# Kernel tuning notes

Hardware: AMD Instinct MI355X
Metric: run time of the kernel (lower is better)

Reference implementation:

```python
import jax, jax.numpy as jnp
import numpy as np

N, E, B, D, L, IN, H = 50000, 800000, 64, 64, 4, 7, 4


def _leaky(x, s=0.2):
    return jnp.where(x >= 0, x, s * x)


def _layernorm(x, g, b, eps=1e-5):
    mu = x.mean(-1, keepdims=True)
    v = ((x - mu) ** 2).mean(-1, keepdims=True)
    return (x - mu) * jax.lax.rsqrt(v + eps) * g + b


def _forward(x, edge_index, batch,
             enc_W, enc_b,
             gat_Wl, gat_Wr, gat_att, gat_b,
             ln_g, ln_b, ffn_W1, ffn_b1, ffn_W2, ffn_b2,
             n2g_W1, n2g_b1, n2g_W2, n2g_b2,
             g2n_W1, g2n_b1, g2n_W2, g2n_b2,
             dec_W1, dec_b1, dec_W2, dec_b2):
    n = x.shape[0]
    loops = jnp.arange(n, dtype=edge_index.dtype)
    src = jnp.concatenate([edge_index[0], loops])  # PyG add_self_loops=True
    dst = jnp.concatenate([edge_index[1], loops])

    h = x @ enc_W + enc_b  # encoder [N, D]
    for l in range(L):
        # ---- GATv2Conv(heads=4, concat=False), eval mode (dropout off) ----
        xl = (h @ gat_Wl[l]).reshape(n, H, D)  # source transform (lin_l)
        xr = (h @ gat_Wr[l]).reshape(n, H, D)  # target transform (lin_r)
        s = xl[src] + xr[dst]                              # [Et, H, D]
        e = jnp.sum(_leaky(s) * gat_att[l], axis=-1)       # [Et, H]
        m = jax.ops.segment_max(e, dst, num_segments=n)
        a = jnp.exp(e - m[dst])
        denom = jax.ops.segment_sum(a, dst, num_segments=n)
        a = a / (denom[dst] + 1e-16)                       # segment softmax
        out = jax.ops.segment_sum(a[..., None] * xl[src], dst, num_segments=n)
        out = out.mean(axis=1) + gat_b[l]                  # head average + bias
        # ---- residual + LayerNorm + FFN ----
        h2 = _layernorm(h + out, ln_g[l], ln_b[l])
        h = h2 + (_leaky(h2 @ ffn_W1[l] + ffn_b1[l]) @ ffn_W2[l] + ffn_b2[l])
        # ---- GlobalContextLayer ----
        lat = jax.nn.gelu(h @ n2g_W1[l] + n2g_b1[l]) @ n2g_W2[l] + n2g_b2[l]
        cnt = jax.ops.segment_sum(jnp.ones((n, 1), h.dtype), batch, num_segments=B)
        gmean = jax.ops.segment_sum(lat, batch, num_segments=B) / jnp.maximum(cnt, 1.0)
        gmax = jax.ops.segment_max(lat, batch, num_segments=B)
        gl = jnp.concatenate([gmean, gmax], axis=1)        # [B, 2D]
        ctx = jax.nn.gelu(gl @ g2n_W1[l] + g2n_b1[l]) @ g2n_W2[l] + g2n_b2[l]
        h = h + ctx[batch]
    return jax.nn.gelu(h @ dec_W1 + dec_b1) @ dec_W2 + dec_b2  # [N, 2]


def setup_inputs() -> dict:
    key = jax.random.key(0)
    ks = jax.random.split(key, 16)
    f = lambda i, s: jax.random.normal(ks[i], s, dtype=jnp.float32) * 0.1
    z = lambda s: jnp.zeros(s, jnp.float32)
    return dict(
        x=jax.random.normal(ks[0], (N, IN), dtype=jnp.float32),
        edge_index=jax.random.randint(ks[1], (2, E), 0, N, dtype=jnp.int32),
        batch=jnp.sort(jax.random.randint(ks[2], (N,), 0, B, dtype=jnp.int32)),
        enc_W=f(3, (IN, D)), enc_b=z((D,)),
        gat_Wl=f(4, (L, D, H * D)), gat_Wr=f(5, (L, D, H * D)),
        gat_att=f(6, (L, H, D)), gat_b=z((L, D)),
        ln_g=jnp.ones((L, D), jnp.float32), ln_b=z((L, D)),
        ffn_W1=f(7, (L, D, 2 * D)), ffn_b1=z((L, 2 * D)),
        ffn_W2=f(8, (L, 2 * D, D)), ffn_b2=z((L, D)),
        n2g_W1=f(9, (L, D, D)), n2g_b1=z((L, D)),
        n2g_W2=f(10, (L, D, D)), n2g_b2=z((L, D)),
        g2n_W1=f(11, (L, 2 * D, D)), g2n_b1=z((L, D)),
        g2n_W2=f(12, (L, D, D)), g2n_b2=z((L, D)),
        dec_W1=f(13, (D, D)), dec_b1=z((D,)),
        dec_W2=f(14, (D, 2)), dec_b2=z((2,)),
    )


def reference(x, edge_index, batch, enc_W, enc_b, gat_Wl, gat_Wr, gat_att, gat_b,
              ln_g, ln_b, ffn_W1, ffn_b1, ffn_W2, ffn_b2,
              n2g_W1, n2g_b1, n2g_W2, n2g_b2,
              g2n_W1, g2n_b1, g2n_W2, g2n_b2,
              dec_W1, dec_b1, dec_W2, dec_b2):
    return _forward(x, edge_index, batch, enc_W, enc_b, gat_Wl, gat_Wr, gat_att, gat_b,
                    ln_g, ln_b, ffn_W1, ffn_b1, ffn_W2, ffn_b2,
                    n2g_W1, n2g_b1, n2g_W2, n2g_b2,
                    g2n_W1, g2n_b1, g2n_W2, g2n_b2,
                    dec_W1, dec_b1, dec_W2, dec_b2)
```

## Files before the change

kernel.cpp:

```cpp
#include <hip/hip_runtime.h>
#include <hip/hip_bf16.h>
#include <math.h>

#define NN 50000
#define EE 800000
#define BBATCH 64
#define DDIM 64
#define NLAYER 4
#define NIN 7
#define NHEAD 4

typedef __attribute__((ext_vector_type(8))) short short8v;
typedef __attribute__((ext_vector_type(4))) float f32x4;

static __device__ __forceinline__ float wave_sum(float v) {
#pragma unroll
  for (int m = 32; m > 0; m >>= 1) v += __shfl_xor(v, m, 64);
  return v;
}

static __device__ __forceinline__ float gelu_t(float x) {
  float z = 0.7978845608f * (x + 0.044715f * x * x * x);
  float t = 2.f / (1.f + __expf(-2.f * z)) - 1.f;
  return 0.5f * x * (1.f + t);
}

static __device__ __forceinline__ unsigned short f2b(float v) {
  __hip_bfloat16 b = __float2bfloat16(v);
  return *reinterpret_cast<unsigned short*>(&b);
}

static __device__ __forceinline__ unsigned fkey(float x) {
  unsigned u = __builtin_bit_cast(unsigned, x);
  return (u >> 31) ? ~u : (u | 0x80000000u);
}
static __device__ __forceinline__ float fkey_inv(unsigned k) {
  unsigned u = (k & 0x80000000u) ? (k ^ 0x80000000u) : ~k;
  return __builtin_bit_cast(float, u);
}

template <int CTRL>
static __device__ __forceinline__ float dppf(float v) {
  int x = __builtin_amdgcn_mov_dpp(__builtin_bit_cast(int, v), CTRL, 0xF, 0xF, true);
  return __builtin_bit_cast(float, x);
}

static __device__ __forceinline__ void unpack8(uint4 u, float* xs) {
  unsigned int w[4] = {u.x, u.y, u.z, u.w};
#pragma unroll
  for (int k = 0; k < 4; k++) {
    xs[2 * k]     = __builtin_bit_cast(float, w[k] << 16);
    xs[2 * k + 1] = __builtin_bit_cast(float, w[k] & 0xFFFF0000u);
  }
}

__global__ void k_init_cnt(int* cnt, int n) {
  int i = blockIdx.x * blockDim.x + threadIdx.x;
  if (i < n) cnt[i] = 1;
}

__global__ void k_count_edges(const int* __restrict__ dst, int e, int* cnt) {
  int i = blockIdx.x * blockDim.x + threadIdx.x;
  if (i < e) atomicAdd(&cnt[dst[i]], 1);
}

__global__ void k_scan_bsum(const int* __restrict__ cnt, int n, int* bsum) {
  __shared__ int red[256];
  int b = blockIdx.x, t = threadIdx.x;
  int s = 0;
  for (int i = b * 1024 + t; i < (b + 1) * 1024; i += 256)
    if (i < n) s += cnt[i];
  red[t] = s;
  __syncthreads();
  for (int o = 128; o > 0; o >>= 1) {
    if (t < o) red[t] += red[t + o];
    __syncthreads();
  }
  if (t == 0) bsum[b] = red[0];
}

__global__ void k_scan_offsets(int* bsum, int nb) {
  if (threadIdx.x == 0 && blockIdx.x == 0) {
    int acc = 0;
    for (int i = 0; i < nb; i++) { int v = bsum[i]; bsum[i] = acc; acc += v; }
  }
}

__global__ void k_scan_final(const int* __restrict__ cnt, int n,
                             const int* __restrict__ bsum, int* indptr) {
  __shared__ int lds[256];
  int b = blockIdx.x, t = threadIdx.x;
  int base = b * 1024;
  int v[4];
  int s = 0;
#pragma unroll
  for (int j = 0; j < 4; j++) {
    int i = base + t * 4 + j;
    v[j] = (i < n) ? cnt[i] : 0;
    s += v[j];
  }
  lds[t] = s;
  __syncthreads();
  for (int o = 1; o < 256; o <<= 1) {
    int x = (t >= o) ? lds[t - o] : 0;
    __syncthreads();
    lds[t] += x;
    __syncthreads();
  }
  int run = bsum[b] + lds[t] - s;
#pragma unroll
  for (int j = 0; j < 4; j++) {
    int i = base + t * 4 + j;
    if (i <= n) indptr[i] = run;
    run += v[j];
  }
}

__global__ void k_csr_self(const int* __restrict__ indptr, int* nxt, int* esrc, int n) {
  int i = blockIdx.x * blockDim.x + threadIdx.x;
  if (i < n) {
    int p = indptr[i];
    esrc[p] = i;
    nxt[i] = p + 1;
  }
}

__global__ void k_csr_fill(const int* __restrict__ src, const int* __restrict__ dst,
                           int e, int* nxt, int* esrc) {
  int i = blockIdx.x * blockDim.x + threadIdx.x;
  if (i < e) {
    int p = atomicAdd(&nxt[dst[i]], 1);
    esrc[p] = src[i];
  }
}

__global__ void k_batch_starts(const int* __restrict__ batch, int n, int nb, int* starts) {
  int i = blockIdx.x * blockDim.x + threadIdx.x;
  if (i >= n) return;
  int b = batch[i];
  if (i == 0) {
    for (int x = 0; x <= b; x++) starts[x] = 0;
  } else {
    int pb = batch[i - 1];
    if (pb != b)
      for (int x = pb + 1; x <= b; x++) starts[x] = i;
  }
  if (i == n - 1) {
    for (int x = b + 1; x <= nb; x++) starts[x] = n;
  }
}

#define SEG_LR (4 * 512 * 64)
#define SEG_F1 (4 * 128 * 64)
#define SEG_F2 (4 * 64 * 128)
#define SEG_N  (4 * 64 * 64)
#define SEG_D  (64 * 64)
#define WPREP_TOTAL (SEG_LR + SEG_F1 + SEG_F2 + 2 * SEG_N + SEG_D)
__global__ void k_wprep_all(const float* __restrict__ Wl, const float* __restrict__ Wr,
                            const float* __restrict__ F1, const float* __restrict__ F2,
                            const float* __restrict__ N1, const float* __restrict__ N2,
                            const float* __restrict__ D1,
                            unsigned short* __restrict__ wLR, unsigned short* __restrict__ wF1,
                            unsigned short* __restrict__ wF2, unsigned short* __restrict__ wN1,
                            unsigned short* __restrict__ wN2, unsigned short* __restrict__ wD1) {
  int idx = blockIdx.x * blockDim.x + threadIdx.x;
  if (idx < SEG_LR) {
    int l = idx / (512 * 64), rem = idx % (512 * 64);
    int c = rem / 64, k = rem % 64;
    float v = (c < 256) ? Wl[(size_t)l * 64 * 256 + k * 256 + c]
                        : Wr[(size_t)l * 64 * 256 + k * 256 + (c - 256)];
    wLR[idx] = f2b(v);
    return;
  }
  idx -= SEG_LR;
  if (idx < SEG_F1) {
    int l = idx / (128 * 64), rem = idx % (128 * 64);
    int c = rem / 64, k = rem % 64;
    wF1[idx] = f2b(F1[(size_t)l * 64 * 128 + k * 128 + c]);
    return;
  }
  idx -= SEG_F1;
  if (idx < SEG_F2) {
    int l = idx / (64 * 128), rem = idx % (64 * 128);
    int c = rem / 128, k = rem % 128;
    wF2[idx] = f2b(F2[(size_t)l * 128 * 64 + k * 64 + c]);
    return;
  }
  idx -= SEG_F2;
  if (idx < SEG_N) {
    int l = idx / (64 * 64), rem = idx % (64 * 64);
    int c = rem / 64, k = rem % 64;
    wN1[idx] = f2b(N1[(size_t)l * 64 * 64 + k * 64 + c]);
    return;
  }
  idx -= SEG_N;
  if (idx < SEG_N) {
    int l = idx / (64 * 64), rem = idx % (64 * 64);
    int c = rem / 64, k = rem % 64;
    wN2[idx] = f2b(N2[(size_t)l * 64 * 64 + k * 64 + c]);
    return;
  }
  idx -= SEG_N;
  if (idx < SEG_D) {
    int c = idx / 64, k = idx % 64;
    wD1[idx] = f2b(D1[k * 64 + c]);
  }
}

__global__ void k_encoder(const float* __restrict__ x, const float* __restrict__ W,
                          const float* __restrict__ bias, float* __restrict__ h,
                          unsigned short* __restrict__ hb, int n) {
  int idx = blockIdx.x * blockDim.x + threadIdx.x;
  if (idx >= n * 64) return;
  int i = idx >> 6, d = idx & 63;
  float acc = bias[d];
#pragma unroll
  for (int k = 0; k < NIN; k++) acc += x[i * NIN + k] * W[k * 64 + d];
  h[idx] = acc;
  hb[idx] = f2b(acc);
}

template <int K, int ACT, bool RES, bool BIAS, bool OUTF, bool OUTB>
__global__ __launch_bounds__(256) void k_mgemm(const unsigned short* __restrict__ A,
                                               const unsigned short* __restrict__ Wt,
                                               const float* __restrict__ bias,
                                               const float* __restrict__ res,
                                               float* __restrict__ C,
                                               unsigned short* __restrict__ Cb,
                                               int n, int Co) {
  constexpr int NF = K / 32;
  const int lane = threadIdx.x & 63, wave = threadIdx.x >> 6;
  const int row0 = blockIdx.x * 64 + wave * 16;
  const int c0 = blockIdx.y * 64;
  const int karow = (lane >> 4) * 8;
  const int arow = row0 + (lane & 15);
  const size_t abase = (size_t)(arow < n ? arow : 0) * K + karow;

  short8v a[NF];
#pragma unroll
  for (int f = 0; f < NF; f++)
    a[f] = *(const short8v*)(A + abase + f * 32);

  f32x4 acc[4];
#pragma unroll
  for (int cc = 0; cc < 4; cc++) {
    const int c = c0 + cc * 16 + (lane & 15);
    f32x4 t = {0.f, 0.f, 0.f, 0.f};
#pragma unroll
    for (int f = 0; f < NF; f++) {
      short8v b = *(const short8v*)(Wt + (size_t)c * K + f * 32 + karow);
      t = __builtin_amdgcn_mfma_f32_16x16x32_bf16(a[f], b, t, 0, 0, 0);
    }
    acc[cc] = t;
  }

#pragma unroll
  for (int cc = 0; cc < 4; cc++) {
    const int c = c0 + cc * 16 + (lane & 15);
    const float bv = BIAS ? bias[c] : 0.f;
#pragma unroll
    for (int r = 0; r < 4; r++) {
      const int row = row0 + (lane >> 4) * 4 + r;
      if (row < n) {
        float v = acc[cc][r] + bv;
        if (ACT == 1) v = fmaxf(v, 0.2f * v);
        else if (ACT == 2) v = gelu_t(v);
        if (RES) v += res[(size_t)row * Co + c];
        if (OUTF) C[(size_t)row * Co + c] = v;
        if (OUTB) Cb[(size_t)row * Co + c] = f2b(v);
      }
    }
  }
}

__global__ __launch_bounds__(256) void k_ffn(const unsigned short* __restrict__ A,
                                             const unsigned short* __restrict__ W1t,
                                             const float* __restrict__ b1,
                                             const unsigned short* __restrict__ W2t,
                                             const float* __restrict__ b2,
                                             const float* __restrict__ res,
                                             float* __restrict__ C,
                                             unsigned short* __restrict__ Cb, int n) {
  __shared__ unsigned short tl[4][16 * 136];
  const int lane = threadIdx.x & 63, wave = threadIdx.x >> 6;
  const int row0 = blockIdx.x * 64 + wave * 16;
  const int karow = (lane >> 4) * 8;
  const int arow = row0 + (lane & 15);
  const size_t abase = (size_t)(arow < n ? arow : 0) * 64 + karow;
  short8v a0 = *(const short8v*)(A + abase);
  short8v a1 = *(const short8v*)(A + abase + 32);

#pragma unroll
  for (int cc = 0; cc < 8; cc++) {
    const int c = cc * 16 + (lane & 15);
    f32x4 t = {0.f, 0.f, 0.f, 0.f};
    t = __builtin_amdgcn_mfma_f32_16x16x32_bf16(a0, *(const short8v*)(W1t + (size_t)c * 64 + karow), t, 0, 0, 0);
    t = __builtin_amdgcn_mfma_f32_16x16x32_bf16(a1, *(const short8v*)(W1t + (size_t)c * 64 + 32 + karow), t, 0, 0, 0);
    const float bv = b1[c];
#pragma unroll
    for (int r = 0; r < 4; r++) {
      float v = t[r] + bv;
      v = fmaxf(v, 0.2f * v);
      int rr = (lane >> 4) * 4 + r;
      tl[wave][rr * 136 + c] = f2b(v);
    }
  }
  __syncthreads();

  short8v a2[4];
#pragma unroll
  for (int f = 0; f < 4; f++)
    a2[f] = *(const short8v*)(&tl[wave][(lane & 15) * 136 + f * 32 + karow]);

#pragma unroll
  for (int cc = 0; cc < 4; cc++) {
    const int c = cc * 16 + (lane & 15);
    f32x4 t = {0.f, 0.f, 0.f, 0.f};
#pragma unroll
    for (int f = 0; f < 4; f++)
      t = __builtin_amdgcn_mfma_f32_16x16x32_bf16(a2[f], *(const short8v*)(W2t + (size_t)c * 128 + f * 32 + karow), t, 0, 0, 0);
    const float bv = b2[c];
#pragma unroll
    for (int r = 0; r < 4; r++) {
      const int row = row0 + (lane >> 4) * 4 + r;
      if (row < n) {
        float v = t[r] + bv + res[(size_t)row * 64 + c];
        C[(size_t)row * 64 + c] = v;
        Cb[(size_t)row * 64 + c] = f2b(v);
      }
    }
  }
}

__global__ __launch_bounds__(256) void k_n2g(const unsigned short* __restrict__ A,
                                             const unsigned short* __restrict__ W1t,
                                             const float* __restrict__ b1,
                                             const unsigned short* __restrict__ W2t,
                                             const float* __restrict__ b2,
                                             const int* __restrict__ batch,
                                             float* __restrict__ psum,
                                             unsigned int* __restrict__ pmax, int n) {
  __shared__ unsigned short tl[4][16 * 72];
  __shared__ float s_sum[64];
  __shared__ unsigned s_max[64];
  const int lane = threadIdx.x & 63, wave = threadIdx.x >> 6;
  const int row0b = blockIdx.x * 64;
  const int row0 = row0b + wave * 16;
  const int karow = (lane >> 4) * 8;
  const int arow = row0 + (lane & 15);
  const size_t abase = (size_t)(arow < n ? arow : 0) * 64 + karow;
  if (threadIdx.x < 64) { s_sum[threadIdx.x] = 0.f; s_max[threadIdx.x] = 0u; }
  short8v a0 = *(const short8v*)(A + abase);
  short8v a1 = *(const short8v*)(A + abase + 32);

#pragma unroll
  for (int cc = 0; cc < 4; cc++) {
    const int c = cc * 16 + (lane & 15);
    f32x4 t = {0.f, 0.f, 0.f, 0.f};
    t = __builtin_amdgcn_mfma_f32_16x16x32_bf16(a0, *(const short8v*)(W1t + (size_t)c * 64 + karow), t, 0, 0, 0);
    t = __builtin_amdgcn_mfma_f32_16x16x32_bf16(a1, *(const short8v*)(W1t + (size_t)c * 64 + 32 + karow), t, 0, 0, 0);
    const float bv = b1[c];
#pragma unroll
    for (int r = 0; r < 4; r++) {
      int rr = (lane >> 4) * 4 + r;
      tl[wave][rr * 72 + c] = f2b(gelu_t(t[r] + bv));
    }
  }
  __syncthreads();

  short8v a2[2];
#pragma unroll
  for (int f = 0; f < 2; f++)
    a2[f] = *(const short8v*)(&tl[wave][(lane & 15) * 72 + f * 32 + karow]);

  float pv[4][4];
#pragma unroll
  for (int cc = 0; cc < 4; cc++) {
    const int c = cc * 16 + (lane & 15);
    f32x4 t = {0.f, 0.f, 0.f, 0.f};
    t = __builtin_amdgcn_mfma_f32_16x16x32_bf16(a2[0], *(const short8v*)(W2t + (size_t)c * 64 + karow), t, 0, 0, 0);
    t = __builtin_amdgcn_mfma_f32_16x16x32_bf16(a2[1], *(const short8v*)(W2t + (size_t)c * 64 + 32 + karow), t, 0, 0, 0);
    const float bv = b2[c];
#pragma unroll
    for (int r = 0; r < 4; r++) pv[cc][r] = t[r] + bv;
  }

  const int blo = batch[row0b];
  const int last = row0b + 63 < n ? row0b + 63 : n - 1;
  const int bhi = batch[last];
  if (blo == bhi && row0b + 63 < n) {
#pragma unroll
    for (int cc = 0; cc < 4; cc++) {
      const int c = cc * 16 + (lane & 15);
      float s = pv[cc][0] + pv[cc][1] + pv[cc][2] + pv[cc][3];
      float mx = fmaxf(fmaxf(pv[cc][0], pv[cc][1]), fmaxf(pv[cc][2], pv[cc][3]));
      atomicAdd(&s_sum[c], s);
      atomicMax(&s_max[c], fkey(mx));
    }
    __syncthreads();
    if (threadIdx.x < 64) {
      atomicAdd(&psum[blo * 64 + threadIdx.x], s_sum[threadIdx.x]);
      atomicMax(&pmax[blo * 64 + threadIdx.x], s_max[threadIdx.x]);
    }
  } else {
#pragma unroll
    for (int cc = 0; cc < 4; cc++) {
      const int c = cc * 16 + (lane & 15);
#pragma unroll
      for (int r = 0; r < 4; r++) {
        const int row = row0 + (lane >> 4) * 4 + r;
        if (row < n) {
          const int b = batch[row];
          atomicAdd(&psum[b * 64 + c], pv[cc][r]);
          atomicMax(&pmax[b * 64 + c], fkey(pv[cc][r]));
        }
      }
    }
  }
}

__global__ __launch_bounds__(256) void k_gat(const unsigned short* __restrict__ xlr,
                                             const float* __restrict__ att,
                                             const float* __restrict__ gbias,
                                             const float* __restrict__ lng,
                                             const float* __restrict__ lnb,
                                             const float* __restrict__ h,
                                             const int* __restrict__ indptr,
                                             const int* __restrict__ esrc,
                                             float* __restrict__ h2,
                                             unsigned short* __restrict__ h2b, int n) {
  const int wave = threadIdx.x >> 6, lane = threadIdx.x & 63;
  const int node = blockIdx.x * 4 + wave;
  if (node >= n) return;
  const int q = lane >> 4, r = lane & 15;
  const int c = r & 3;
  const int doff = (r >> 2) * 64 + c * 16;

  float xr_d[16], att_d[16];
  {
    const uint4* xp = (const uint4*)(xlr + (size_t)node * 512 + 256 + doff);
    uint4 u0 = xp[0], u1 = xp[1];
    unpack8(u0, xr_d);
    unpack8(u1, xr_d + 8);
    const float4* ap = (const float4*)(att + doff);
#pragma unroll
    for (int k = 0; k < 4; k++) {
      float4 a = ap[k];
      att_d[4 * k] = a.x; att_d[4 * k + 1] = a.y;
      att_d[4 * k + 2] = a.z; att_d[4 * k + 3] = a.w;
    }
  }

  float acc[16] = {};
  float den = 0.f;
  const int beg = indptr[node], end = indptr[node + 1];

  int j0 = beg + q;
  int s_cur = esrc[(j0 < end) ? j0 : beg];
  const uint4* xp0 = (const uint4*)(xlr + (size_t)s_cur * 512 + doff);
  uint4 u0 = xp0[0], u1 = xp0[1];
  int jn1 = beg + 4 + q;
  int s_nxt = esrc[(jn1 < end && beg + 4 < end) ? jn1 : beg];

  for (int jb = beg; jb < end; jb += 4) {
    const uint4 cu0 = u0, cu1 = u1;
    const bool cvalid = (jb + q) < end;
    if (jb + 4 < end) {
      const uint4* xpn = (const uint4*)(xlr + (size_t)s_nxt * 512 + doff);
      u0 = xpn[0];
      u1 = xpn[1];
      if (jb + 8 < end) {
        const int jn = jb + 8 + q;
        s_nxt = esrc[(jn < end) ? jn : beg];
      }
    }
    float xs[16];
    unpack8(cu0, xs);
    unpack8(cu1, xs + 8);
    float p0 = 0.f, p1 = 0.f, p2 = 0.f, p3 = 0.f;
#pragma unroll
    for (int k = 0; k < 4; k++) {
      float t0 = xs[4 * k + 0] + xr_d[4 * k + 0]; t0 = fmaxf(t0, 0.2f * t0); p0 = fmaf(t0, att_d[4 * k + 0], p0);
      float t1 = xs[4 * k + 1] + xr_d[4 * k + 1]; t1 = fmaxf(t1, 0.2f * t1); p1 = fmaf(t1, att_d[4 * k + 1], p1);
      float t2 = xs[4 * k + 2] + xr_d[4 * k + 2]; t2 = fmaxf(t2, 0.2f * t2); p2 = fmaf(t2, att_d[4 * k + 2], p2);
      float t3 = xs[4 * k + 3] + xr_d[4 * k + 3]; t3 = fmaxf(t3, 0.2f * t3); p3 = fmaf(t3, att_d[4 * k + 3], p3);
    }
    float p = (p0 + p1) + (p2 + p3);
    p += dppf<0xB1>(p);
    p += dppf<0x4E>(p);
    const float pw = cvalid ? __expf(fminf(p, 60.f)) : 0.f;
    den += pw;
#pragma unroll
    for (int d = 0; d < 16; d++) acc[d] = fmaf(pw, xs[d], acc[d]);
  }

  den += __shfl_xor(den, 16, 64);
  den += __shfl_xor(den, 32, 64);
#pragma unroll
  for (int d = 0; d < 16; d++) {
    acc[d] += __shfl_xor(acc[d], 16, 64);
    acc[d] += __shfl_xor(acc[d], 32, 64);
  }

  const float rden = 0.25f / (den + 1e-16f);
  float y[16];
  float s4 = 0.f;
  const float4* hp = (const float4*)(h + (size_t)node * 64 + c * 16);
  const float4* gp = (const float4*)(gbias + c * 16);
#pragma unroll
  for (int k = 0; k < 4; k++) {
    float4 hv = hp[k], gv = gp[k];
    float hf[4] = {hv.x, hv.y, hv.z, hv.w};
    float gf[4] = {gv.x, gv.y, gv.z, gv.w};
#pragma unroll
    for (int d2 = 0; d2 < 4; d2++) {
      int d = 4 * k + d2;
      float v = acc[d] * rden;
      v += dppf<0x124>(v);
      v += dppf<0x128>(v);
      y[d] = hf[d2] + v + gf[d2];
      s4 += y[d];
    }
  }

  const float mu = wave_sum(s4) * (1.f / 1024.f);
  float v4 = 0.f;
  float dv[16];
#pragma unroll
  for (int d = 0; d < 16; d++) {
    dv[d] = y[d] - mu;
    v4 += dv[d] * dv[d];
  }
  const float var = wave_sum(v4) * (1.f / 1024.f);
  const float rstd = rsqrtf(var + 1e-5f);

  if (lane < 4) {
    float4* outp = (float4*)(h2 + (size_t)node * 64 + lane * 16);
    uint2* outb = (uint2*)(h2b + (size_t)node * 64 + lane * 16);
    const float4* lgp = (const float4*)(lng + lane * 16);
    const float4* lbp = (const float4*)(lnb + lane * 16);
#pragma unroll
    for (int k = 0; k < 4; k++) {
      float4 g = lgp[k], b = lbp[k];
      float o0 = dv[4 * k + 0] * rstd * g.x + b.x;
      float o1 = dv[4 * k + 1] * rstd * g.y + b.y;
      float o2 = dv[4 * k + 2] * rstd * g.z + b.z;
      float o3 = dv[4 * k + 3] * rstd * g.w + b.w;
      float4 of; of.x = o0; of.y = o1; of.z = o2; of.w = o3;
      outp[k] = of;
      uint2 pk;
      pk.x = (unsigned int)f2b(o0) | ((unsigned int)f2b(o1) << 16);
      pk.y = (unsigned int)f2b(o2) | ((unsigned int)f2b(o3) << 16);
      outb[k] = pk;
    }
  }
}

__global__ void k_ctx2(const float* __restrict__ psum, const unsigned int* __restrict__ pmax,
                       const int* __restrict__ starts,
                       const float* __restrict__ W1, const float* __restrict__ b1,
                       const float* __restrict__ W2, const float* __restrict__ b2,
                       float* __restrict__ ctx) {
  int b = blockIdx.x;
  int t = threadIdx.x;
  __shared__ float g[128], tt[64];
  int cnt = starts[b + 1] - starts[b];
  if (t < 64) {
    g[t] = psum[b * 64 + t] / fmaxf((float)cnt, 1.0f);
  } else {
    g[t] = fkey_inv(pmax[b * 64 + (t - 64)]);
  }
  __syncthreads();
  if (t < 64) {
    float acc = b1[t];
    for (int k = 0; k < 128; k++) acc += g[k] * W1[k * 64 + t];
    tt[t] = gelu_t(acc);
  }
  __syncthreads();
  if (t < 64) {
    float acc2 = b2[t];
    for (int k = 0; k < 64; k++) acc2 += tt[k] * W2[k * 64 + t];
    ctx[b * 64 + t] = acc2;
  }
}

__global__ void k_add_ctx(float* __restrict__ h, unsigned short* __restrict__ hb,
                          const float* __restrict__ ctx,
                          const int* __restrict__ batch, int n) {
  int idx = blockIdx.x * blockDim.x + threadIdx.x;
  if (idx >= n * 64) return;
  int i = idx >> 6, d = idx & 63;
  float v = h[idx] + ctx[batch[i] * 64 + d];
  h[idx] = v;
  hb[idx] = f2b(v);
}

__global__ __launch_bounds__(256) void k_dec(const unsigned short* __restrict__ A,
                                             const unsigned short* __restrict__ W1t,
                                             const float* __restrict__ b1,
                                             const float* __restrict__ W2,
                                             const float* __restrict__ b2,
                                             float* __restrict__ out, int n) {
  const int lane = threadIdx.x & 63, wave = threadIdx.x >> 6;
  const int row0 = blockIdx.x * 64 + wave * 16;
  const int karow = (lane >> 4) * 8;
  const int arow = row0 + (lane & 15);
  const size_t abase = (size_t)(arow < n ? arow : 0) * 64 + karow;
  short8v a0 = *(const short8v*)(A + abase);
  short8v a1 = *(const short8v*)(A + abase + 32);

  float o0[4] = {}, o1[4] = {};
#pragma unroll
  for (int cc = 0; cc < 4; cc++) {
    const int cidx = cc * 16 + (lane & 15);
    f32x4 t = {0.f, 0.f, 0.f, 0.f};
    t = __builtin_amdgcn_mfma_f32_16x16x32_bf16(a0, *(const short8v*)(W1t + (size_t)cidx * 64 + karow), t, 0, 0, 0);
    t = __builtin_amdgcn_mfma_f32_16x16x32_bf16(a1, *(const short8v*)(W1t + (size_t)cidx * 64 + 32 + karow), t, 0, 0, 0);
    const float bv = b1[cidx];
    const float w0 = W2[cidx * 2 + 0], w1 = W2[cidx * 2 + 1];
#pragma unroll
    for (int r = 0; r < 4; r++) {
      float v = gelu_t(t[r] + bv);
      o0[r] = fmaf(v, w0, o0[r]);
      o1[r] = fmaf(v, w1, o1[r]);
    }
  }
#pragma unroll
  for (int m = 1; m < 16; m <<= 1) {
#pragma unroll
    for (int r = 0; r < 4; r++) {
      o0[r] += __shfl_xor(o0[r], m, 64);
      o1[r] += __shfl_xor(o1[r], m, 64);
    }
  }
  if ((lane & 15) == 0) {
#pragma unroll
    for (int r = 0; r < 4; r++) {
      const int row = row0 + (lane >> 4) * 4 + r;
      if (row < n) {
        out[2 * row] = o0[r] + b2[0];
        out[2 * row + 1] = o1[r] + b2[1];
      }
    }
  }
}

extern "C" void kernel_launch(void* const* d_in, const int* in_sizes, int n_in,
                              void* d_out, int out_size, void* d_ws, size_t ws_size,
                              hipStream_t stream) {
  const float* x = (const float*)d_in[0];
  const int* ei = (const int*)d_in[1];
  const int* batch = (const int*)d_in[2];
  const float* enc_W = (const float*)d_in[3];
  const float* enc_b = (const float*)d_in[4];
  const float* gat_Wl = (const float*)d_in[5];
  const float* gat_Wr = (const float*)d_in[6];
  const float* gat_att = (const float*)d_in[7];
  const float* gat_b = (const float*)d_in[8];
  const float* ln_g = (const float*)d_in[9];
  const float* ln_b = (const float*)d_in[10];
  const float* ffn_W1 = (const float*)d_in[11];
  const float* ffn_b1 = (const float*)d_in[12];
  const float* ffn_W2 = (const float*)d_in[13];
  const float* ffn_b2 = (const float*)d_in[14];
  const float* n2g_W1 = (const float*)d_in[15];
  const float* n2g_b1 = (const float*)d_in[16];
  const float* n2g_W2 = (const float*)d_in[17];
  const float* n2g_b2 = (const float*)d_in[18];
  const float* g2n_W1 = (const float*)d_in[19];
  const float* g2n_b1 = (const float*)d_in[20];
  const float* g2n_W2 = (const float*)d_in[21];
  const float* g2n_b2 = (const float*)d_in[22];
  const float* dec_W1 = (const float*)d_in[23];
  const float* dec_b1 = (const float*)d_in[24];
  const float* dec_W2 = (const float*)d_in[25];
  const float* dec_b2 = (const float*)d_in[26];

  const int N = NN, E = EE;
  const int* e_src = ei;
  const int* e_dst = ei + E;

  float* h = (float*)d_ws;
  float* h2 = h + (size_t)N * 64;
  float* ctx = h2 + (size_t)N * 64;
  float* psum = ctx + BBATCH * 64;
  unsigned int* pmax = (unsigned int*)(psum + BBATCH * 64);
  int* cnt = (int*)(pmax + BBATCH * 64);
  int* indptr = cnt + N;
  int* esrc = indptr + N + 1;
  int* bsum = esrc + (E + N);
  int* starts = bsum + 64;
  size_t off = (size_t)(starts + BBATCH + 1) - (size_t)d_ws;
  off = (off + 15) & ~(size_t)15;
  unsigned short* hb = (unsigned short*)((char*)d_ws + off);
  unsigned short* h2b = hb + (size_t)N * 64;
  unsigned short* xlr = h2b + (size_t)N * 64;
  unsigned short* wLR = xlr + (size_t)N * 512;
  unsigned short* wF1 = wLR + SEG_LR;
  unsigned short* wF2 = wF1 + SEG_F1;
  unsigned short* wN1 = wF2 + SEG_F2;
  unsigned short* wN2 = wN1 + SEG_N;
  unsigned short* wD1 = wN2 + SEG_N;

  const int TPB = 256;
  const int NBLK_SCAN = (N + 1 + 1023) / 1024;

  hipLaunchKernelGGL(k_wprep_all, dim3((WPREP_TOTAL + 255) / 256), dim3(256), 0, stream,
                     gat_Wl, gat_Wr, ffn_W1, ffn_W2, n2g_W1, n2g_W2, dec_W1,
                     wLR, wF1, wF2, wN1, wN2, wD1);

  hipLaunchKernelGGL(k_init_cnt, dim3((N + TPB - 1) / TPB), dim3(TPB), 0, stream, cnt, N);
  hipLaunchKernelGGL(k_count_edges, dim3((E + TPB - 1) / TPB), dim3(TPB), 0, stream, e_dst, E, cnt);
  hipLaunchKernelGGL(k_scan_bsum, dim3(NBLK_SCAN), dim3(256), 0, stream, cnt, N, bsum);
  hipLaunchKernelGGL(k_scan_offsets, dim3(1), dim3(64), 0, stream, bsum, NBLK_SCAN);
  hipLaunchKernelGGL(k_scan_final, dim3(NBLK_SCAN), dim3(256), 0, stream, cnt, N, bsum, indptr);
  hipLaunchKernelGGL(k_csr_self, dim3((N + TPB - 1) / TPB), dim3(TPB), 0, stream, indptr, cnt, esrc, N);
  hipLaunchKernelGGL(k_csr_fill, dim3((E + TPB - 1) / TPB), dim3(TPB), 0, stream, e_src, e_dst, E, cnt, esrc);
  hipLaunchKernelGGL(k_batch_starts, dim3((N + TPB - 1) / TPB), dim3(TPB), 0, stream, batch, N, BBATCH, starts);

  hipLaunchKernelGGL(k_encoder, dim3((N * 64 + TPB - 1) / TPB), dim3(TPB), 0, stream,
                     x, enc_W, enc_b, h, hb, N);

  const int GN = (N + 63) / 64;

  for (int l = 0; l < NLAYER; l++) {
    const unsigned short* LRt = wLR + (size_t)l * 512 * 64;
    const unsigned short* F1t = wF1 + (size_t)l * 128 * 64;
    const unsigned short* F2t = wF2 + (size_t)l * 64 * 128;
    const unsigned short* N1t = wN1 + (size_t)l * 64 * 64;
    const unsigned short* N2t = wN2 + (size_t)l * 64 * 64;
    const float* attl = gat_att + (size_t)l * 256;
    const float* gbl = gat_b + (size_t)l * 64;
    const float* lngl = ln_g + (size_t)l * 64;
    const float* lnbl = ln_b + (size_t)l * 64;
    const float* fb1 = ffn_b1 + (size_t)l * 128;
    const float* fb2 = ffn_b2 + (size_t)l * 64;
    const float* nb1 = n2g_b1 + (size_t)l * 64;
    const float* nb2 = n2g_b2 + (size_t)l * 64;
    const float* gW1 = g2n_W1 + (size_t)l * 128 * 64;
    const float* gb1 = g2n_b1 + (size_t)l * 64;
    const float* gW2 = g2n_W2 + (size_t)l * 64 * 64;
    const float* gb2 = g2n_b2 + (size_t)l * 64;

    hipLaunchKernelGGL((k_mgemm<64, 0, false, false, false, true>), dim3(GN, 8), dim3(256), 0, stream,
                       hb, LRt, nullptr, nullptr, nullptr, xlr, N, 512);
    hipLaunchKernelGGL(k_gat, dim3((N + 3) / 4), dim3(256), 0, stream,
                       xlr, attl, gbl, lngl, lnbl, h, indptr, esrc, h2, h2b, N);
    hipLaunchKernelGGL(k_ffn, dim3(GN), dim3(256), 0, stream,
                       h2b, F1t, fb1, F2t, fb2, h2, h, hb, N);
    hipMemsetAsync(psum, 0, BBATCH * 64 * (sizeof(float) + sizeof(unsigned int)), stream);
    hipLaunchKernelGGL(k_n2g, dim3(GN), dim3(256), 0, stream,
                       hb, N1t, nb1, N2t, nb2, batch, psum, pmax, N);
    hipLaunchKernelGGL(k_ctx2, dim3(BBATCH), dim3(128), 0, stream,
                       psum, pmax, starts, gW1, gb1, gW2, gb2, ctx);
    hipLaunchKernelGGL(k_add_ctx, dim3((N * 64 + TPB - 1) / TPB), dim3(TPB), 0, stream,
                       h, hb, ctx, batch, N);
  }

  hipLaunchKernelGGL(k_dec, dim3(GN), dim3(256), 0, stream,
                     hb, wD1, dec_b1, dec_W2, dec_b2, (float*)d_out, N);
}
```

Measured before the change: 869.4 us.

## Fuse context add into next-layer consumers and drop separate passes

Removes the k_add_ctx pass by folding the per-graph context vector into the next layer's xlr GEMM and GAT residual, and into the decoder. Those kernels now read fp32 h and convert to bf16 on the fly. Also folds the CSR self-loop insertion into the scan kernel, and hoists the per-layer memset into one upfront memset over per-layer psum/pmax buffers. The GAT inner loop is rewritten with packed float2 vector ops. The cost is extra fp32 reads and ctx gathers in the xlr kernel, which runs over 8 column blocks.

```diff
diff --git a/kernel.cpp b/kernel.cpp
--- a/kernel.cpp
+++ b/kernel.cpp
@@ -12,6 +12,7 @@
 
 typedef __attribute__((ext_vector_type(8))) short short8v;
 typedef __attribute__((ext_vector_type(4))) float f32x4;
+typedef __attribute__((ext_vector_type(2))) float v2f;
 
 static __device__ __forceinline__ float wave_sum(float v) {
 #pragma unroll
@@ -45,13 +46,18 @@
   return __builtin_bit_cast(float, x);
 }
 
-static __device__ __forceinline__ void unpack8(uint4 u, float* xs) {
-  unsigned int w[4] = {u.x, u.y, u.z, u.w};
-#pragma unroll
-  for (int k = 0; k < 4; k++) {
-    xs[2 * k]     = __builtin_bit_cast(float, w[k] << 16);
-    xs[2 * k + 1] = __builtin_bit_cast(float, w[k] & 0xFFFF0000u);
-  }
+static __device__ __forceinline__ v2f up2(unsigned w) {
+  v2f r;
+  r.x = __builtin_bit_cast(float, w << 16);
+  r.y = __builtin_bit_cast(float, w & 0xFFFF0000u);
+  return r;
+}
+
+static __device__ __forceinline__ short8v pack8(const float* v) {
+  short8v r;
+#pragma unroll
+  for (int j = 0; j < 8; j++) r[j] = (short)f2b(v[j]);
+  return r;
 }
 
 __global__ void k_init_cnt(int* cnt, int n) {
@@ -86,8 +92,9 @@
   }
 }
 
-__global__ void k_scan_final(const int* __restrict__ cnt, int n,
-                             const int* __restrict__ bsum, int* indptr) {
+__global__ void k_scan_final(int* __restrict__ cnt, int n,
+                             const int* __restrict__ bsum, int* __restrict__ indptr,
+                             int* __restrict__ esrc) {
   __shared__ int lds[256];
   int b = blockIdx.x, t = threadIdx.x;
   int base = b * 1024;
@@ -111,17 +118,14 @@
 #pragma unroll
   for (int j = 0; j < 4; j++) {
     int i = base + t * 4 + j;
-    if (i <= n) indptr[i] = run;
+    if (i < n) {
+      indptr[i] = run;
+      esrc[run] = i;
+      cnt[i] = run + 1;
+    } else if (i == n) {
+      indptr[n] = run;
+    }
     run += v[j];
-  }
-}
-
-__global__ void k_csr_self(const int* __restrict__ indptr, int* nxt, int* esrc, int n) {
-  int i = blockIdx.x * blockDim.x + threadIdx.x;
-  if (i < n) {
-    int p = indptr[i];
-    esrc[p] = i;
-    nxt[i] = p + 1;
   }
 }
 
@@ -208,8 +212,7 @@
 }
 
 __global__ void k_encoder(const float* __restrict__ x, const float* __restrict__ W,
-                          const float* __restrict__ bias, float* __restrict__ h,
-                          unsigned short* __restrict__ hb, int n) {
+                          const float* __restrict__ bias, float* __restrict__ h, int n) {
   int idx = blockIdx.x * blockDim.x + threadIdx.x;
   if (idx >= n * 64) return;
   int i = idx >> 6, d = idx & 63;
@@ -217,58 +220,56 @@
 #pragma unroll
   for (int k = 0; k < NIN; k++) acc += x[i * NIN + k] * W[k * 64 + d];
   h[idx] = acc;
-  hb[idx] = f2b(acc);
-}
-
-template <int K, int ACT, bool RES, bool BIAS, bool OUTF, bool OUTB>
-__global__ __launch_bounds__(256) void k_mgemm(const unsigned short* __restrict__ A,
-                                               const unsigned short* __restrict__ Wt,
-                                               const float* __restrict__ bias,
-                                               const float* __restrict__ res,
-                                               float* __restrict__ C,
-                                               unsigned short* __restrict__ Cb,
-                                               int n, int Co) {
-  constexpr int NF = K / 32;
+}
+
+template <bool CTX>
+__global__ __launch_bounds__(256) void k_xlr(const float* __restrict__ A,
+                                             const float* __restrict__ ctxv,
+                                             const int* __restrict__ batch,
+                                             const unsigned short* __restrict__ Wt,
+                                             unsigned short* __restrict__ Cb, int n) {
   const int lane = threadIdx.x & 63, wave = threadIdx.x >> 6;
   const int row0 = blockIdx.x * 64 + wave * 16;
   const int c0 = blockIdx.y * 64;
   const int karow = (lane >> 4) * 8;
-  const int arow = row0 + (lane & 15);
-  const size_t abase = (size_t)(arow < n ? arow : 0) * K + karow;
-
-  short8v a[NF];
-#pragma unroll
-  for (int f = 0; f < NF; f++)
-    a[f] = *(const short8v*)(A + abase + f * 32);
-
-  f32x4 acc[4];
+  const int arow0 = row0 + (lane & 15);
+  const int arow = arow0 < n ? arow0 : 0;
+  const float* ap = A + (size_t)arow * 64;
+
+  float av[16];
+  {
+    float4 f0 = *(const float4*)(ap + karow);
+    float4 f1 = *(const float4*)(ap + karow + 4);
+    float4 f2 = *(const float4*)(ap + 32 + karow);
+    float4 f3 = *(const float4*)(ap + 32 + karow + 4);
+    av[0] = f0.x; av[1] = f0.y; av[2] = f0.z; av[3] = f0.w;
+    av[4] = f1.x; av[5] = f1.y; av[6] = f1.z; av[7] = f1.w;
+    av[8] = f2.x; av[9] = f2.y; av[10] = f2.z; av[11] = f2.w;
+    av[12] = f3.x; av[13] = f3.y; av[14] = f3.z; av[15] = f3.w;
+    if (CTX) {
+      const float* cp = ctxv + batch[arow] * 64;
+      float4 c0v = *(const float4*)(cp + karow);
+      float4 c1v = *(const float4*)(cp + karow + 4);
+      float4 c2v = *(const float4*)(cp + 32 + karow);
+      float4 c3v = *(const float4*)(cp + 32 + karow + 4);
+      av[0] += c0v.x; av[1] += c0v.y; av[2] += c0v.z; av[3] += c0v.w;
+      av[4] += c1v.x; av[5] += c1v.y; av[6] += c1v.z; av[7] += c1v.w;
+      av[8] += c2v.x; av[9] += c2v.y; av[10] += c2v.z; av[11] += c2v.w;
+      av[12] += c3v.x; av[13] += c3v.y; av[14] += c3v.z; av[15] += c3v.w;
+    }
+  }
+  short8v a0 = pack8(av), a1 = pack8(av + 8);
+
 #pragma unroll
   for (int cc = 0; cc < 4; cc++) {
     const int c = c0 + cc * 16 + (lane & 15);
     f32x4 t = {0.f, 0.f, 0.f, 0.f};
-#pragma unroll
-    for (int f = 0; f < NF; f++) {
-      short8v b = *(const short8v*)(Wt + (size_t)c * K + f * 32 + karow);
-      t = __builtin_amdgcn_mfma_f32_16x16x32_bf16(a[f], b, t, 0, 0, 0);
-    }
-    acc[cc] = t;
-  }
-
-#pragma unroll
-  for (int cc = 0; cc < 4; cc++) {
-    const int c = c0 + cc * 16 + (lane & 15);
-    const float bv = BIAS ? bias[c] : 0.f;
+    t = __builtin_amdgcn_mfma_f32_16x16x32_bf16(a0, *(const short8v*)(Wt + (size_t)c * 64 + karow), t, 0, 0, 0);
+    t = __builtin_amdgcn_mfma_f32_16x16x32_bf16(a1, *(const short8v*)(Wt + (size_t)c * 64 + 32 + karow), t, 0, 0, 0);
 #pragma unroll
     for (int r = 0; r < 4; r++) {
       const int row = row0 + (lane >> 4) * 4 + r;
-      if (row < n) {
-        float v = acc[cc][r] + bv;
-        if (ACT == 1) v = fmaxf(v, 0.2f * v);
-        else if (ACT == 2) v = gelu_t(v);
-        if (RES) v += res[(size_t)row * Co + c];
-        if (OUTF) C[(size_t)row * Co + c] = v;
-        if (OUTB) Cb[(size_t)row * Co + c] = f2b(v);
-      }
+      if (row < n) Cb[(size_t)row * 512 + c] = f2b(t[r]);
     }
   }
 }
@@ -419,12 +420,15 @@
   }
 }
 
+template <bool CTX>
 __global__ __launch_bounds__(256) void k_gat(const unsigned short* __restrict__ xlr,
                                              const float* __restrict__ att,
                                              const float* __restrict__ gbias,
                                              const float* __restrict__ lng,
                                              const float* __restrict__ lnb,
                                              const float* __restrict__ h,
+                                             const float* __restrict__ ctxv,
+                                             const int* __restrict__ batch,
                                              const int* __restrict__ indptr,
                                              const int* __restrict__ esrc,
                                              float* __restrict__ h2,
@@ -436,22 +440,23 @@
   const int c = r & 3;
   const int doff = (r >> 2) * 64 + c * 16;
 
-  float xr_d[16], att_d[16];
+  v2f xr2[8], at2[8];
   {
     const uint4* xp = (const uint4*)(xlr + (size_t)node * 512 + 256 + doff);
     uint4 u0 = xp[0], u1 = xp[1];
-    unpack8(u0, xr_d);
-    unpack8(u1, xr_d + 8);
+    unsigned w[8] = {u0.x, u0.y, u0.z, u0.w, u1.x, u1.y, u1.z, u1.w};
+#pragma unroll
+    for (int j = 0; j < 8; j++) xr2[j] = up2(w[j]);
     const float4* ap = (const float4*)(att + doff);
 #pragma unroll
     for (int k = 0; k < 4; k++) {
       float4 a = ap[k];
-      att_d[4 * k] = a.x; att_d[4 * k + 1] = a.y;
-      att_d[4 * k + 2] = a.z; att_d[4 * k + 3] = a.w;
-    }
-  }
-
-  float acc[16] = {};
+      at2[2 * k].x = a.x; at2[2 * k].y = a.y;
+      at2[2 * k + 1].x = a.z; at2[2 * k + 1].y = a.w;
+    }
+  }
+
+  v2f acc2[8] = {};
   float den = 0.f;
   const int beg = indptr[node], end = indptr[node + 1];
 
@@ -474,32 +479,37 @@
         s_nxt = esrc[(jn < end) ? jn : beg];
       }
     }
-    float xs[16];
-    unpack8(cu0, xs);
-    unpack8(cu1, xs + 8);
-    float p0 = 0.f, p1 = 0.f, p2 = 0.f, p3 = 0.f;
-#pragma unroll
-    for (int k = 0; k < 4; k++) {
-      float t0 = xs[4 * k + 0] + xr_d[4 * k + 0]; t0 = fmaxf(t0, 0.2f * t0); p0 = fmaf(t0, att_d[4 * k + 0], p0);
-      float t1 = xs[4 * k + 1] + xr_d[4 * k + 1]; t1 = fmaxf(t1, 0.2f * t1); p1 = fmaf(t1, att_d[4 * k + 1], p1);
-      float t2 = xs[4 * k + 2] + xr_d[4 * k + 2]; t2 = fmaxf(t2, 0.2f * t2); p2 = fmaf(t2, att_d[4 * k + 2], p2);
-      float t3 = xs[4 * k + 3] + xr_d[4 * k + 3]; t3 = fmaxf(t3, 0.2f * t3); p3 = fmaf(t3, att_d[4 * k + 3], p3);
-    }
-    float p = (p0 + p1) + (p2 + p3);
+    unsigned w[8] = {cu0.x, cu0.y, cu0.z, cu0.w, cu1.x, cu1.y, cu1.z, cu1.w};
+    v2f xs2[8];
+#pragma unroll
+    for (int j = 0; j < 8; j++) xs2[j] = up2(w[j]);
+    v2f p2 = {0.f, 0.f};
+#pragma unroll
+    for (int j = 0; j < 8; j++) {
+      v2f t = xs2[j] + xr2[j];
+      t = __builtin_elementwise_max(t, t * 0.2f);
+      p2 = __builtin_elementwise_fma(t, at2[j], p2);
+    }
+    float p = p2.x + p2.y;
     p += dppf<0xB1>(p);
     p += dppf<0x4E>(p);
     const float pw = cvalid ? __expf(fminf(p, 60.f)) : 0.f;
     den += pw;
-#pragma unroll
-    for (int d = 0; d < 16; d++) acc[d] = fmaf(pw, xs[d], acc[d]);
-  }
+    v2f pwv = {pw, pw};
+#pragma unroll
+    for (int j = 0; j < 8; j++) acc2[j] = __builtin_elementwise_fma(pwv, xs2[j], acc2[j]);
+  }
+
+  float accf[16];
+#pragma unroll
+  for (int j = 0; j < 8; j++) { accf[2 * j] = acc2[j].x; accf[2 * j + 1] = acc2[j].y; }
 
   den += __shfl_xor(den, 16, 64);
   den += __shfl_xor(den, 32, 64);
 #pragma unroll
   for (int d = 0; d < 16; d++) {
-    acc[d] += __shfl_xor(acc[d], 16, 64);
-    acc[d] += __shfl_xor(acc[d], 32, 64);
+    accf[d] += __shfl_xor(accf[d], 16, 64);
+    accf[d] += __shfl_xor(accf[d], 32, 64);
   }
 
   const float rden = 0.25f / (den + 1e-16f);
@@ -507,15 +517,20 @@
   float s4 = 0.f;
   const float4* hp = (const float4*)(h + (size_t)node * 64 + c * 16);
   const float4* gp = (const float4*)(gbias + c * 16);
+  const float4* cp = CTX ? (const float4*)(ctxv + batch[node] * 64 + c * 16) : nullptr;
 #pragma unroll
   for (int k = 0; k < 4; k++) {
     float4 hv = hp[k], gv = gp[k];
+    if (CTX) {
+      float4 cv = cp[k];
+      hv.x += cv.x; hv.y += cv.y; hv.z += cv.z; hv.w += cv.w;
+    }
     float hf[4] = {hv.x, hv.y, hv.z, hv.w};
     float gf[4] = {gv.x, gv.y, gv.z, gv.w};
 #pragma unroll
     for (int d2 = 0; d2 < 4; d2++) {
       int d = 4 * k + d2;
-      float v = acc[d] * rden;
+      float v = accf[d] * rden;
       v += dppf<0x124>(v);
       v += dppf<0x128>(v);
       y[d] = hf[d2] + v + gf[d2];
@@ -584,18 +599,9 @@
   }
 }
 
-__global__ void k_add_ctx(float* __restrict__ h, unsigned short* __restrict__ hb,
-                          const float* __restrict__ ctx,
-                          const int* __restrict__ batch, int n) {
-  int idx = blockIdx.x * blockDim.x + threadIdx.x;
-  if (idx >= n * 64) return;
-  int i = idx >> 6, d = idx & 63;
-  float v = h[idx] + ctx[batch[i] * 64 + d];
-  h[idx] = v;
-  hb[idx] = f2b(v);
-}
-
-__global__ __launch_bounds__(256) void k_dec(const unsigned short* __restrict__ A,
+__global__ __launch_bounds__(256) void k_dec(const float* __restrict__ A,
+                                             const float* __restrict__ ctxv,
+                                             const int* __restrict__ batch,
                                              const unsigned short* __restrict__ W1t,
                                              const float* __restrict__ b1,
                                              const float* __restrict__ W2,
@@ -604,10 +610,27 @@
   const int lane = threadIdx.x & 63, wave = threadIdx.x >> 6;
   const int row0 = blockIdx.x * 64 + wave * 16;
   const int karow = (lane >> 4) * 8;
-  const int arow = row0 + (lane & 15);
-  const size_t abase = (size_t)(arow < n ? arow : 0) * 64 + karow;
-  short8v a0 = *(const short8v*)(A + abase);
-  short8v a1 = *(const short8v*)(A + abase + 32);
+  const int arow0 = row0 + (lane & 15);
+  const int arow = arow0 < n ? arow0 : 0;
+  const float* ap = A + (size_t)arow * 64;
+  const float* cp = ctxv + batch[arow] * 64;
+
+  float av[16];
+  {
+    float4 f0 = *(const float4*)(ap + karow);
+    float4 f1 = *(const float4*)(ap + karow + 4);
+    float4 f2 = *(const float4*)(ap + 32 + karow);
+    float4 f3 = *(const float4*)(ap + 32 + karow + 4);
+    float4 c0v = *(const float4*)(cp + karow);
+    float4 c1v = *(const float4*)(cp + karow + 4);
+    float4 c2v = *(const float4*)(cp + 32 + karow);
+    float4 c3v = *(const float4*)(cp + 32 + karow + 4);
+    av[0] = f0.x + c0v.x; av[1] = f0.y + c0v.y; av[2] = f0.z + c0v.z; av[3] = f0.w + c0v.w;
+    av[4] = f1.x + c1v.x; av[5] = f1.y + c1v.y; av[6] = f1.z + c1v.z; av[7] = f1.w + c1v.w;
+    av[8] = f2.x + c2v.x; av[9] = f2.y + c2v.y; av[10] = f2.z + c2v.z; av[11] = f2.w + c2v.w;
+    av[12] = f3.x + c3v.x; av[13] = f3.y + c3v.y; av[14] = f3.z + c3v.z; av[15] = f3.w + c3v.w;
+  }
+  short8v a0 = pack8(av), a1 = pack8(av + 8);
 
   float o0[4] = {}, o1[4] = {};
 #pragma unroll
@@ -683,9 +706,9 @@
   float* h = (float*)d_ws;
   float* h2 = h + (size_t)N * 64;
   float* ctx = h2 + (size_t)N * 64;
-  float* psum = ctx + BBATCH * 64;
-  unsigned int* pmax = (unsigned int*)(psum + BBATCH * 64);
-  int* cnt = (int*)(pmax + BBATCH * 64);
+  float* psum_all = ctx + BBATCH * 64;
+  unsigned int* pmax_all = (unsigned int*)(psum_all + 4 * BBATCH * 64);
+  int* cnt = (int*)(pmax_all + 4 * BBATCH * 64);
   int* indptr = cnt + N;
   int* esrc = indptr + N + 1;
   int* bsum = esrc + (E + N);
@@ -713,13 +736,14 @@
   hipLaunchKernelGGL(k_count_edges, dim3((E + TPB - 1) / TPB), dim3(TPB), 0, stream, e_dst, E, cnt);
   hipLaunchKernelGGL(k_scan_bsum, dim3(NBLK_SCAN), dim3(256), 0, stream, cnt, N, bsum);
   hipLaunchKernelGGL(k_scan_offsets, dim3(1), dim3(64), 0, stream, bsum, NBLK_SCAN);
-  hipLaunchKernelGGL(k_scan_final, dim3(NBLK_SCAN), dim3(256), 0, stream, cnt, N, bsum, indptr);
-  hipLaunchKernelGGL(k_csr_self, dim3((N + TPB - 1) / TPB), dim3(TPB), 0, stream, indptr, cnt, esrc, N);
+  hipLaunchKernelGGL(k_scan_final, dim3(NBLK_SCAN), dim3(256), 0, stream, cnt, N, bsum, indptr, esrc);
   hipLaunchKernelGGL(k_csr_fill, dim3((E + TPB - 1) / TPB), dim3(TPB), 0, stream, e_src, e_dst, E, cnt, esrc);
   hipLaunchKernelGGL(k_batch_starts, dim3((N + TPB - 1) / TPB), dim3(TPB), 0, stream, batch, N, BBATCH, starts);
 
+  hipMemsetAsync(psum_all, 0, 4 * BBATCH * 64 * (sizeof(float) + sizeof(unsigned int)), stream);
+
   hipLaunchKernelGGL(k_encoder, dim3((N * 64 + TPB - 1) / TPB), dim3(TPB), 0, stream,
-                     x, enc_W, enc_b, h, hb, N);
+                     x, enc_W, enc_b, h, N);
 
   const int GN = (N + 63) / 64;
 
@@ -741,22 +765,29 @@
     const float* gb1 = g2n_b1 + (size_t)l * 64;
     const float* gW2 = g2n_W2 + (size_t)l * 64 * 64;
     const float* gb2 = g2n_b2 + (size_t)l * 64;
-
-    hipLaunchKernelGGL((k_mgemm<64, 0, false, false, false, true>), dim3(GN, 8), dim3(256), 0, stream,
-                       hb, LRt, nullptr, nullptr, nullptr, xlr, N, 512);
-    hipLaunchKernelGGL(k_gat, dim3((N + 3) / 4), dim3(256), 0, stream,
-                       xlr, attl, gbl, lngl, lnbl, h, indptr, esrc, h2, h2b, N);
+    float* psumL = psum_all + (size_t)l * BBATCH * 64;
+    unsigned int* pmaxL = pmax_all + (size_t)l * BBATCH * 64;
+
+    if (l == 0)
+      hipLaunchKernelGGL((k_xlr<false>), dim3(GN, 8), dim3(256), 0, stream,
+                         h, nullptr, nullptr, LRt, xlr, N);
+    else
+      hipLaunchKernelGGL((k_xlr<true>), dim3(GN, 8), dim3(256), 0, stream,
+                         h, ctx, batch, LRt, xlr, N);
+    if (l == 0)
+      hipLaunchKernelGGL((k_gat<false>), dim3((N + 3) / 4), dim3(256), 0, stream,
+                         xlr, attl, gbl, lngl, lnbl, h, nullptr, nullptr, indptr, esrc, h2, h2b, N);
+    else
+      hipLaunchKernelGGL((k_gat<true>), dim3((N + 3) / 4), dim3(256), 0, stream,
+                         xlr, attl, gbl, lngl, lnbl, h, ctx, batch, indptr, esrc, h2, h2b, N);
     hipLaunchKernelGGL(k_ffn, dim3(GN), dim3(256), 0, stream,
                        h2b, F1t, fb1, F2t, fb2, h2, h, hb, N);
-    hipMemsetAsync(psum, 0, BBATCH * 64 * (sizeof(float) + sizeof(unsigned int)), stream);
     hipLaunchKernelGGL(k_n2g, dim3(GN), dim3(256), 0, stream,
-                       hb, N1t, nb1, N2t, nb2, batch, psum, pmax, N);
+                       hb, N1t, nb1, N2t, nb2, batch, psumL, pmaxL, N);
     hipLaunchKernelGGL(k_ctx2, dim3(BBATCH), dim3(128), 0, stream,
-                       psum, pmax, starts, gW1, gb1, gW2, gb2, ctx);
-    hipLaunchKernelGGL(k_add_ctx, dim3((N * 64 + TPB - 1) / TPB), dim3(TPB), 0, stream,
-                       h, hb, ctx, batch, N);
+                       psumL, pmaxL, starts, gW1, gb1, gW2, gb2, ctx);
   }
 
   hipLaunchKernelGGL(k_dec, dim3(GN), dim3(256), 0, stream,
-                     hb, wD1, dec_b1, dec_W2, dec_b2, (float*)d_out, N);
-}
+                     h, ctx, batch, wD1, dec_b1, dec_W2, dec_b2, (float*)d_out, N);
+}
```

After: 879.0 us. About the same (+1.1%).
